# Kernel tuning notes

Hardware: AMD Instinct MI355X
Metric: run time of the kernel (lower is better)

## Reference

```python
import jax, jax.numpy as jnp
import numpy as np

B, N, C, D, H, O = 32, 2048, 16, 128, 128, 128


def setup_inputs():
    key = jax.random.key(0)
    ks = jax.random.split(key, 6)
    childrenList = jax.random.randint(ks[0], (B, N, C), 0, N)
    nodeEmb = jax.random.normal(ks[1], (B, N, D), dtype=jnp.float32)
    std1 = 1.0 / np.sqrt(D)
    W1 = jax.random.normal(ks[2], (3 * D, H), dtype=jnp.float32) * std1
    b1 = jax.random.normal(ks[3], (H,), dtype=jnp.float32) * (2.0 * std1)
    std2 = 1.0 / np.sqrt(H)
    W2 = jax.random.normal(ks[4], (H, O), dtype=jnp.float32) * std2
    b2 = jax.random.normal(ks[5], (O,), dtype=jnp.float32) * (2.0 * std2)
    return {"childrenList": childrenList, "nodeEmb": nodeEmb,
            "W1": W1, "b1": b1, "W2": W2, "b2": b2}


def _gather_feature(children, emb):
    # children: [B,N,C] int (0 = padding/no child), emb: [B,N,D]
    Bx, Nx, Dx = emb.shape
    # index 0 must look up a zero vector (padding child)
    lookup = jnp.concatenate([jnp.zeros((Bx, 1, Dx), emb.dtype), emb[:, 1:, :]], axis=1)
    child_emb = jax.vmap(lambda lu, ch: lu[ch])(lookup, children)      # [B,N,C,D]
    return jnp.concatenate([emb[:, :, None, :], child_emb], axis=2)    # [B,N,C+1,D]


def _conv_weights(children):
    # TBCNN positional coefficients eta_t / eta_r / eta_l (Mou et al.)
    Bx, Nx, Cx = children.shape
    f32 = jnp.float32
    mask = (children > 0).astype(f32)                                   # [B,N,C]
    t = jnp.concatenate([jnp.ones((Bx, Nx, 1), f32),
                         jnp.zeros((Bx, Nx, Cx), f32)], axis=2)        # parent=1, children=0
    num_sib = jnp.sum(mask, axis=2, keepdims=True)                      # [B,N,1]
    pos = jnp.arange(1, Cx + 1, dtype=f32)                              # 1-based child position
    r_child = jnp.where(num_sib == 1, 0.5 * mask,
                        mask * (pos - 1.0) / jnp.maximum(num_sib - 1.0, 1.0))
    r = jnp.concatenate([jnp.zeros((Bx, Nx, 1), f32), r_child], axis=2)
    full_mask = jnp.concatenate([jnp.ones((Bx, Nx, 1), f32), mask], axis=2)
    l = (1.0 - t) * (1.0 - r) * full_mask
    return jnp.stack([t, r, l], axis=-1)                                # [B,N,C+1,3]


def reference(childrenList, nodeEmb, W1, b1, W2, b2):
    feature = _gather_feature(childrenList, nodeEmb)                    # [B,N,C+1,D]
    weights = _conv_weights(childrenList)                               # [B,N,C+1,3]
    wf = jnp.einsum('bnck,bncd->bnkd', weights, feature)                # [B,N,3,D]
    wf = wf.reshape(wf.shape[0], wf.shape[1], -1)                       # [B,N,3D]
    h = jnp.tanh(wf @ W1 + b1)                                          # [B,N,H]
    pooled = jnp.max(h, axis=1)                                         # [B,H] max-pool over nodes
    out = jnp.tanh(pooled @ W2 + b2)                                    # [B,O]
    half = out.shape[0] // 2
    v1, v2 = out[:half], out[half:]
    eps = 1e-8
    n1 = jnp.maximum(jnp.linalg.norm(v1, axis=1), eps)
    n2 = jnp.maximum(jnp.linalg.norm(v2, axis=1), eps)
    return jnp.sum(v1 * v2, axis=1) / (n1 * n2)                         # [B/2]
```

## Files before the change

kernel.cpp:

```cpp
#include <hip/hip_runtime.h>

#define NB 32
#define NN 2048
#define NC 16
#define ND 128
#define NH 128
#define TM 64
#define NBLK (NB * (NN / TM))

typedef __bf16 bf16x8 __attribute__((ext_vector_type(8)));
typedef float f32x4 __attribute__((ext_vector_type(4)));
typedef float f32x2 __attribute__((ext_vector_type(2)));

__device__ __forceinline__ unsigned short f2bf(float f){
  unsigned u = __float_as_uint(f);
  u = (u + 0x7fffu + ((u >> 16) & 1u)) >> 16;
  return (unsigned short)u;
}
__device__ __forceinline__ unsigned enc_f32(float x){
  unsigned u = __float_as_uint(x);
  return (u & 0x80000000u) ? ~u : (u | 0x80000000u);
}
__device__ __forceinline__ float dec_f32(unsigned u){
  return __uint_as_float((u & 0x80000000u) ? (u & 0x7fffffffu) : ~u);
}
__device__ __forceinline__ unsigned pack4f8(float a, float b, float c, float d){
  int r = __builtin_amdgcn_cvt_pk_fp8_f32(a, b, 0, false);
  r = __builtin_amdgcn_cvt_pk_fp8_f32(c, d, r, true);
  return (unsigned)r;
}

__device__ __forceinline__ void stq(unsigned char* base, int stride, int row, int koff, uint4 u){
  *(uint4*)(base + row * stride + (koff ^ ((row & 7) << 4))) = u;
}
__device__ __forceinline__ void st8(unsigned char* base, int stride, int row, int koff, const float* f){
  uint4 u;
  u.x = (unsigned)f2bf(f[0]) | ((unsigned)f2bf(f[1]) << 16);
  u.y = (unsigned)f2bf(f[2]) | ((unsigned)f2bf(f[3]) << 16);
  u.z = (unsigned)f2bf(f[4]) | ((unsigned)f2bf(f[5]) << 16);
  u.w = (unsigned)f2bf(f[6]) | ((unsigned)f2bf(f[7]) << 16);
  stq(base, stride, row, koff, u);
}
__device__ __forceinline__ void st8p(unsigned char* base, int stride, int row, int koff, const f32x2* p){
  uint4 u;
  u.x = (unsigned)f2bf(p[0][0]) | ((unsigned)f2bf(p[0][1]) << 16);
  u.y = (unsigned)f2bf(p[1][0]) | ((unsigned)f2bf(p[1][1]) << 16);
  u.z = (unsigned)f2bf(p[2][0]) | ((unsigned)f2bf(p[2][1]) << 16);
  u.w = (unsigned)f2bf(p[3][0]) | ((unsigned)f2bf(p[3][1]) << 16);
  stq(base, stride, row, koff, u);
}
__device__ __forceinline__ uint4 ldq(const unsigned char* base, int stride, int row, int koff){
  return *(const uint4*)(base + row * stride + (koff ^ ((row & 7) << 4)));
}

#define OFF_POOLED 0
#define OFF_W1     16384
#define OFF_W2     114688
#define OFF_EMB    147456
#define WS_NEED_F8 (OFF_EMB + (size_t)NB*NN*ND)

__global__ __launch_bounds__(256) void tbcnn_prep(
    const float* __restrict__ nodeEmb, const float* __restrict__ W1,
    const float* __restrict__ W2, unsigned* __restrict__ pooled,
    uint4* __restrict__ w1frag, uint4* __restrict__ w2frag,
    unsigned char* __restrict__ embF8, int doEmb)
{
  const int blk = blockIdx.x;
  const int t = threadIdx.x;
  if (blk < 2048){
    if (!doEmb) return;
    const int chk = ((blk & 7) << 8) | (blk >> 3);
    const int tid = chk * 256 + t;
    const float4* src = (const float4*)nodeEmb;
    float4 v0 = src[tid * 4 + 0];
    float4 v1 = src[tid * 4 + 1];
    float4 v2 = src[tid * 4 + 2];
    float4 v3 = src[tid * 4 + 3];
    uint4 o;
    o.x = pack4f8(v0.x, v0.y, v0.z, v0.w);
    o.y = pack4f8(v1.x, v1.y, v1.z, v1.w);
    o.z = pack4f8(v2.x, v2.y, v2.z, v2.w);
    o.w = pack4f8(v3.x, v3.y, v3.z, v3.w);
    ((uint4*)embF8)[tid] = o;
  } else if (blk < 2072){
    const int tt = (blk - 2048) * 256 + t;
    if (tt < NB * NH) pooled[tt] = 0u;
    const int lane = tt & 63;
    const int rest = tt >> 6;
    const int ks = rest % 12;
    const int cf = rest / 12;
    const int col = (cf >> 1) * 32 + (cf & 1) * 16 + (lane & 15);
    const int k0 = ks * 32 + (lane >> 4) * 8;
    unsigned ps[4];
    #pragma unroll
    for (int p = 0; p < 4; ++p){
      unsigned lo = f2bf(W1[(size_t)(k0 + 2*p) * NH + col]);
      unsigned hi = f2bf(W1[(size_t)(k0 + 2*p + 1) * NH + col]);
      ps[p] = lo | (hi << 16);
    }
    w1frag[tt] = make_uint4(ps[0], ps[1], ps[2], ps[3]);
  } else {
    const int tt = (blk - 2072) * 256 + t;
    const int lane = tt & 63;
    const int rest = tt >> 6;
    const int ks = rest & 3;
    const int cf = rest >> 2;
    const int col = (cf >> 1) * 32 + (cf & 1) * 16 + (lane & 15);
    const int k0 = ks * 32 + (lane >> 4) * 8;
    unsigned ps[4];
    #pragma unroll
    for (int p = 0; p < 4; ++p){
      unsigned lo = f2bf(W2[(size_t)(k0 + 2*p) * NH + col]);
      unsigned hi = f2bf(W2[(size_t)(k0 + 2*p + 1) * NH + col]);
      ps[p] = lo | (hi << 16);
    }
    w2frag[tt] = make_uint4(ps[0], ps[1], ps[2], ps[3]);
  }
}

#define PROCF8(u, p) { \
  f32x2 lo_ = __builtin_amdgcn_cvt_pk_f32_fp8((int)(u), false); \
  f32x2 hi_ = __builtin_amdgcn_cvt_pk_f32_fp8((int)(u), true); \
  aR2[(p)]   += w_r * lo_; aL2[(p)]   += w_l * lo_; \
  aR2[(p)+1] += w_r * hi_; aL2[(p)+1] += w_l * hi_; }

#define ISSUE4(vv, D) { \
  D[0] = *(const uint4*)(embF8 + (rowbase + (unsigned)(vv).x) * ND + d0); \
  D[1] = *(const uint4*)(embF8 + (rowbase + (unsigned)(vv).y) * ND + d0); \
  D[2] = *(const uint4*)(embF8 + (rowbase + (unsigned)(vv).z) * ND + d0); \
  D[3] = *(const uint4*)(embF8 + (rowbase + (unsigned)(vv).w) * ND + d0); }

#define CW(c, idx) \
  const float mk  = ((idx) > 0) ? 1.0f : 0.0f; \
  const float wrc = one_sib ? (0.5f * mk) : (mk * (float)(c) * rdiv); \
  const float wlc = (1.0f - wrc) * mk; \
  const f32x2 w_r = (f32x2){wrc, wrc}; \
  const f32x2 w_l = (f32x2){wlc, wlc};

#define PROC4(g, vv, U) { \
  { CW(4*(g)+0, (vv).x) PROCF8(U[0].x,0) PROCF8(U[0].y,2) PROCF8(U[0].z,4) PROCF8(U[0].w,6) } \
  { CW(4*(g)+1, (vv).y) PROCF8(U[1].x,0) PROCF8(U[1].y,2) PROCF8(U[1].z,4) PROCF8(U[1].w,6) } \
  { CW(4*(g)+2, (vv).z) PROCF8(U[2].x,0) PROCF8(U[2].y,2) PROCF8(U[2].z,4) PROCF8(U[2].w,6) } \
  { CW(4*(g)+3, (vv).w) PROCF8(U[3].x,0) PROCF8(U[3].y,2) PROCF8(U[3].z,4) PROCF8(U[3].w,6) } }

template<bool F8>
__global__ __launch_bounds__(256, 2) void tbcnn_main(
    const int* __restrict__ children, const float* __restrict__ nodeEmb,
    const unsigned char* __restrict__ embF8, const uint4* __restrict__ w1frag,
    unsigned* __restrict__ pooled)
{
  __shared__ __align__(16) unsigned char wf_raw[TM * 768];
  const int j0 = ((blockIdx.x & 7) << 7) | (blockIdx.x >> 3);
  const int b = j0 >> 5;
  const int n0 = (j0 & 31) * TM;
  const int t = threadIdx.x;
  const int lane = t & 63;
  const int w = t >> 6;
  const size_t rowbase = (size_t)b * NN;

  #pragma unroll
  for (int pass = 0; pass < 2; ++pass){
    const int nloc = pass * 32 + (t >> 3);
    const int q = t & 7;
    const int d0 = q * 16;
    const int gn = n0 + nloc;
    const int4* chp4 = (const int4*)(children + (rowbase + gn) * NC);

    const int4 vA = chp4[0], vB = chp4[1], vC = chp4[2], vD = chp4[3];
    int ns = (vA.x > 0) + (vA.y > 0) + (vA.z > 0) + (vA.w > 0)
           + (vB.x > 0) + (vB.y > 0) + (vB.z > 0) + (vB.w > 0)
           + (vC.x > 0) + (vC.y > 0) + (vC.z > 0) + (vC.w > 0)
           + (vD.x > 0) + (vD.y > 0) + (vD.z > 0) + (vD.w > 0);
    const float rdiv = 1.0f / (float)(((ns - 1) > 1) ? (ns - 1) : 1);
    const bool one_sib = (ns == 1);

    if (F8){
      f32x2 aR2[8], aL2[8];
      #pragma unroll
      for (int i = 0; i < 8; ++i){ aR2[i] = (f32x2){0.f,0.f}; aL2[i] = (f32x2){0.f,0.f}; }

      uint4 g0[4], g1[4];
      const uint4 sq = *(const uint4*)(embF8 + (rowbase + gn) * ND + d0);
      ISSUE4(vA, g0)
      ISSUE4(vB, g1)
      __builtin_amdgcn_sched_barrier(0);
      {
        f32x2 sv[8];
        sv[0] = __builtin_amdgcn_cvt_pk_f32_fp8((int)sq.x, false);
        sv[1] = __builtin_amdgcn_cvt_pk_f32_fp8((int)sq.x, true);
        sv[2] = __builtin_amdgcn_cvt_pk_f32_fp8((int)sq.y, false);
        sv[3] = __builtin_amdgcn_cvt_pk_f32_fp8((int)sq.y, true);
        sv[4] = __builtin_amdgcn_cvt_pk_f32_fp8((int)sq.z, false);
        sv[5] = __builtin_amdgcn_cvt_pk_f32_fp8((int)sq.z, true);
        sv[6] = __builtin_amdgcn_cvt_pk_f32_fp8((int)sq.w, false);
        sv[7] = __builtin_amdgcn_cvt_pk_f32_fp8((int)sq.w, true);
        st8p(wf_raw, 768, nloc, 2 * d0,       sv);
        st8p(wf_raw, 768, nloc, 2 * (d0 + 8), sv + 4);
      }
      PROC4(0, vA, g0)
      ISSUE4(vC, g0)
      __builtin_amdgcn_sched_barrier(0);
      PROC4(1, vB, g1)
      ISSUE4(vD, g1)
      __builtin_amdgcn_sched_barrier(0);
      PROC4(2, vC, g0)
      __builtin_amdgcn_sched_barrier(0);
      PROC4(3, vD, g1)

      st8p(wf_raw, 768, nloc, 2 * (ND + d0),         aR2);
      st8p(wf_raw, 768, nloc, 2 * (ND + d0 + 8),     aR2 + 4);
      st8p(wf_raw, 768, nloc, 2 * (2 * ND + d0),     aL2);
      st8p(wf_raw, 768, nloc, 2 * (2 * ND + d0 + 8), aL2 + 4);
    } else {
      const float* sp = nodeEmb + (rowbase + gn) * ND + d0;
      float sv[16];
      #pragma unroll
      for (int j = 0; j < 4; ++j){
        float4 s = *(const float4*)(sp + j * 4);
        sv[j*4+0]=s.x; sv[j*4+1]=s.y; sv[j*4+2]=s.z; sv[j*4+3]=s.w;
      }
      st8(wf_raw, 768, nloc, 2 * d0, sv);
      st8(wf_raw, 768, nloc, 2 * (d0 + 8), sv + 8);
      float aR[16], aL[16];
      #pragma unroll
      for (int i = 0; i < 16; ++i){ aR[i] = 0.0f; aL[i] = 0.0f; }
      const int4 vs[4] = {vA, vB, vC, vD};
      #pragma unroll
      for (int c4 = 0; c4 < 4; ++c4){
        int cidx[4] = {vs[c4].x, vs[c4].y, vs[c4].z, vs[c4].w};
        #pragma unroll
        for (int jj = 0; jj < 4; ++jj){
          const int c = c4 * 4 + jj;
          const int idx = cidx[jj];
          const float mk  = (idx > 0) ? 1.0f : 0.0f;
          const float wrc = one_sib ? (0.5f * mk) : (mk * (float)c * rdiv);
          const float wlc = (1.0f - wrc) * mk;
          const float* cp = nodeEmb + (rowbase + idx) * ND + d0;
          #pragma unroll
          for (int j = 0; j < 4; ++j){
            float4 u = *(const float4*)(cp + j * 4);
            aR[j*4+0] += wrc * u.x; aL[j*4+0] += wlc * u.x;
            aR[j*4+1] += wrc * u.y; aL[j*4+1] += wlc * u.y;
            aR[j*4+2] += wrc * u.z; aL[j*4+2] += wlc * u.z;
            aR[j*4+3] += wrc * u.w; aL[j*4+3] += wlc * u.w;
          }
        }
      }
      st8(wf_raw, 768, nloc, 2 * (ND + d0),         aR);
      st8(wf_raw, 768, nloc, 2 * (ND + d0 + 8),     aR + 8);
      st8(wf_raw, 768, nloc, 2 * (2 * ND + d0),     aL);
      st8(wf_raw, 768, nloc, 2 * (2 * ND + d0 + 8), aL + 8);
    }
  }
  __syncthreads();

  {
    f32x4 acc[4][2];
    #pragma unroll
    for (int rf = 0; rf < 4; ++rf){
      acc[rf][0] = (f32x4){0.f, 0.f, 0.f, 0.f};
      acc[rf][1] = (f32x4){0.f, 0.f, 0.f, 0.f};
    }
    #pragma unroll 4
    for (int ks = 0; ks < 12; ++ks){
      bf16x8 B0 = __builtin_bit_cast(bf16x8, w1frag[((w * 2 + 0) * 12 + ks) * 64 + lane]);
      bf16x8 B1 = __builtin_bit_cast(bf16x8, w1frag[((w * 2 + 1) * 12 + ks) * 64 + lane]);
      const int koff = ks * 64 + ((lane >> 4) << 4);
      #pragma unroll
      for (int rf = 0; rf < 4; ++rf){
        const int row = rf * 16 + (lane & 15);
        bf16x8 a = __builtin_bit_cast(bf16x8, ldq(wf_raw, 768, row, koff));
        acc[rf][0] = __builtin_amdgcn_mfma_f32_16x16x32_bf16(a, B0, acc[rf][0], 0, 0, 0);
        acc[rf][1] = __builtin_amdgcn_mfma_f32_16x16x32_bf16(a, B1, acc[rf][1], 0, 0, 0);
      }
    }

    float m0 = -3.0e38f, m1 = -3.0e38f;
    #pragma unroll
    for (int rf = 0; rf < 4; ++rf)
      #pragma unroll
      for (int i = 0; i < 4; ++i){
        m0 = fmaxf(m0, acc[rf][0][i]);
        m1 = fmaxf(m1, acc[rf][1][i]);
      }
    m0 = fmaxf(m0, __shfl_xor(m0, 16, 64));
    m0 = fmaxf(m0, __shfl_xor(m0, 32, 64));
    m1 = fmaxf(m1, __shfl_xor(m1, 16, 64));
    m1 = fmaxf(m1, __shfl_xor(m1, 32, 64));
    if (lane < 16){
      atomicMax(pooled + b * NH + w * 32 + lane,      enc_f32(m0));
      atomicMax(pooled + b * NH + w * 32 + 16 + lane, enc_f32(m1));
    }
  }
}

__global__ __launch_bounds__(256) void tbcnn_final(
    const unsigned* __restrict__ pooled, const float* __restrict__ b1,
    const uint4* __restrict__ w2frag, const float* __restrict__ b2,
    float* __restrict__ out)
{
  __shared__ __align__(16) unsigned char hls[NB * 256];
  __shared__ float os[NB * NH];
  const int t = threadIdx.x;
  const int lane = t & 63;
  const int w = t >> 6;

  {
    const int row = t >> 3;
    const int q = t & 7;
    const int d0 = q * 16;
    const unsigned* pp = pooled + row * NH + d0;
    const float* bp = b1 + d0;
    float hv[16];
    #pragma unroll
    for (int j = 0; j < 16; ++j) hv[j] = tanhf(dec_f32(pp[j]) + bp[j]);
    st8(hls, 256, row, 2 * d0, hv);
    st8(hls, 256, row, 2 * (d0 + 8), hv + 8);
  }
  __syncthreads();
  {
    f32x4 acc[2][2];
    #pragma unroll
    for (int rf = 0; rf < 2; ++rf){
      acc[rf][0] = (f32x4){0.f,0.f,0.f,0.f};
      acc[rf][1] = (f32x4){0.f,0.f,0.f,0.f};
    }
    #pragma unroll
    for (int ks = 0; ks < 4; ++ks){
      bf16x8 B0 = __builtin_bit_cast(bf16x8, w2frag[((w * 2 + 0) * 4 + ks) * 64 + lane]);
      bf16x8 B1 = __builtin_bit_cast(bf16x8, w2frag[((w * 2 + 1) * 4 + ks) * 64 + lane]);
      const int koff = ks * 64 + ((lane >> 4) << 4);
      #pragma unroll
      for (int rf = 0; rf < 2; ++rf){
        bf16x8 a = __builtin_bit_cast(bf16x8, ldq(hls, 256, rf * 16 + (lane & 15), koff));
        acc[rf][0] = __builtin_amdgcn_mfma_f32_16x16x32_bf16(a, B0, acc[rf][0], 0, 0, 0);
        acc[rf][1] = __builtin_amdgcn_mfma_f32_16x16x32_bf16(a, B1, acc[rf][1], 0, 0, 0);
      }
    }
    #pragma unroll
    for (int rf = 0; rf < 2; ++rf)
      #pragma unroll
      for (int cf = 0; cf < 2; ++cf){
        const int col = w * 32 + cf * 16 + (lane & 15);
        const float bias = b2[col];
        #pragma unroll
        for (int i = 0; i < 4; ++i){
          const int r = rf * 16 + (lane >> 4) * 4 + i;
          os[r * NH + col] = tanhf(acc[rf][cf][i] + bias);
        }
      }
  }
  __syncthreads();
  if (t < 16){
    float s12 = 0.f, s11 = 0.f, s22 = 0.f;
    #pragma unroll 4
    for (int d = 0; d < NH; ++d){
      float a = os[t * NH + d];
      float c = os[(t + 16) * NH + d];
      s12 += a * c; s11 += a * a; s22 += c * c;
    }
    float n1 = fmaxf(sqrtf(s11), 1e-8f);
    float n2 = fmaxf(sqrtf(s22), 1e-8f);
    out[t] = s12 / (n1 * n2);
  }
}

extern "C" void kernel_launch(void* const* d_in, const int* in_sizes, int n_in,
                              void* d_out, int out_size, void* d_ws, size_t ws_size,
                              hipStream_t stream)
{
  const int*   children = (const int*)d_in[0];
  const float* nodeEmb  = (const float*)d_in[1];
  const float* W1       = (const float*)d_in[2];
  const float* b1       = (const float*)d_in[3];
  const float* W2       = (const float*)d_in[4];
  const float* b2       = (const float*)d_in[5];
  float* out = (float*)d_out;

  unsigned* pooled      = (unsigned*)((char*)d_ws + OFF_POOLED);
  uint4* w1frag         = (uint4*)((char*)d_ws + OFF_W1);
  uint4* w2frag         = (uint4*)((char*)d_ws + OFF_W2);
  unsigned char* embF8  = (unsigned char*)((char*)d_ws + OFF_EMB);

  const bool f8 = (ws_size >= WS_NEED_F8);

  tbcnn_prep<<<2080, 256, 0, stream>>>(nodeEmb, W1, W2, pooled, w1frag, w2frag, embF8, f8 ? 1 : 0);
  if (f8)
    tbcnn_main<true><<<NBLK, 256, 0, stream>>>(children, nodeEmb, embF8, w1frag, pooled);
  else
    tbcnn_main<false><<<NBLK, 256, 0, stream>>>(children, nodeEmb, embF8, w1frag, pooled);
  tbcnn_final<<<1, 256, 0, stream>>>(pooled, b1, w2frag, b2, out);
}
```

Baseline: 40.91 us.

## Use 512-thread blocks so each node row and each output tile gets its own thread/wave

Doubles the block size of the main kernel from 256 to 512 threads. The two-pass gather loop becomes a single pass, with each thread handling one node-row slice. The MFMA stage now uses 8 waves that each compute one 16-column output slice instead of 4 waves computing two. This aims to expose more parallelism and latency hiding within a block, but launch bounds drop to one block per CU and per-thread register pressure changes.

After: 41.26 us. Within noise of the previous version (+0.9%).

```diff
diff --git a/kernel.cpp b/kernel.cpp
--- a/kernel.cpp
+++ b/kernel.cpp
@@ -144,7 +144,7 @@
   { CW(4*(g)+3, (vv).w) PROCF8(U[3].x,0) PROCF8(U[3].y,2) PROCF8(U[3].z,4) PROCF8(U[3].w,6) } }
 
 template<bool F8>
-__global__ __launch_bounds__(256, 2) void tbcnn_main(
+__global__ __launch_bounds__(512, 1) void tbcnn_main(
     const int* __restrict__ children, const float* __restrict__ nodeEmb,
     const unsigned char* __restrict__ embF8, const uint4* __restrict__ w1frag,
     unsigned* __restrict__ pooled)
@@ -158,9 +158,8 @@
   const int w = t >> 6;
   const size_t rowbase = (size_t)b * NN;
 
-  #pragma unroll
-  for (int pass = 0; pass < 2; ++pass){
-    const int nloc = pass * 32 + (t >> 3);
+  {
+    const int nloc = t >> 3;
     const int q = t & 7;
     const int d0 = q * 16;
     const int gn = n0 + nloc;
@@ -255,42 +254,31 @@
   __syncthreads();
 
   {
-    f32x4 acc[4][2];
-    #pragma unroll
-    for (int rf = 0; rf < 4; ++rf){
-      acc[rf][0] = (f32x4){0.f, 0.f, 0.f, 0.f};
-      acc[rf][1] = (f32x4){0.f, 0.f, 0.f, 0.f};
-    }
+    f32x4 acc[4];
+    #pragma unroll
+    for (int rf = 0; rf < 4; ++rf) acc[rf] = (f32x4){0.f, 0.f, 0.f, 0.f};
     #pragma unroll 4
     for (int ks = 0; ks < 12; ++ks){
-      bf16x8 B0 = __builtin_bit_cast(bf16x8, w1frag[((w * 2 + 0) * 12 + ks) * 64 + lane]);
-      bf16x8 B1 = __builtin_bit_cast(bf16x8, w1frag[((w * 2 + 1) * 12 + ks) * 64 + lane]);
+      bf16x8 B0 = __builtin_bit_cast(bf16x8, w1frag[(w * 12 + ks) * 64 + lane]);
       const int koff = ks * 64 + ((lane >> 4) << 4);
       #pragma unroll
       for (int rf = 0; rf < 4; ++rf){
         const int row = rf * 16 + (lane & 15);
         bf16x8 a = __builtin_bit_cast(bf16x8, ldq(wf_raw, 768, row, koff));
-        acc[rf][0] = __builtin_amdgcn_mfma_f32_16x16x32_bf16(a, B0, acc[rf][0], 0, 0, 0);
-        acc[rf][1] = __builtin_amdgcn_mfma_f32_16x16x32_bf16(a, B1, acc[rf][1], 0, 0, 0);
-      }
-    }
-
-    float m0 = -3.0e38f, m1 = -3.0e38f;
+        acc[rf] = __builtin_amdgcn_mfma_f32_16x16x32_bf16(a, B0, acc[rf], 0, 0, 0);
+      }
+    }
+
+    float m0 = -3.0e38f;
     #pragma unroll
     for (int rf = 0; rf < 4; ++rf)
       #pragma unroll
-      for (int i = 0; i < 4; ++i){
-        m0 = fmaxf(m0, acc[rf][0][i]);
-        m1 = fmaxf(m1, acc[rf][1][i]);
-      }
+      for (int i = 0; i < 4; ++i)
+        m0 = fmaxf(m0, acc[rf][i]);
     m0 = fmaxf(m0, __shfl_xor(m0, 16, 64));
     m0 = fmaxf(m0, __shfl_xor(m0, 32, 64));
-    m1 = fmaxf(m1, __shfl_xor(m1, 16, 64));
-    m1 = fmaxf(m1, __shfl_xor(m1, 32, 64));
-    if (lane < 16){
-      atomicMax(pooled + b * NH + w * 32 + lane,      enc_f32(m0));
-      atomicMax(pooled + b * NH + w * 32 + 16 + lane, enc_f32(m1));
-    }
+    if (lane < 16)
+      atomicMax(pooled + b * NH + w * 16 + lane, enc_f32(m0));
   }
 }
 
@@ -386,8 +374,8 @@
 
   tbcnn_prep<<<2080, 256, 0, stream>>>(nodeEmb, W1, W2, pooled, w1frag, w2frag, embF8, f8 ? 1 : 0);
   if (f8)
-    tbcnn_main<true><<<NBLK, 256, 0, stream>>>(children, nodeEmb, embF8, w1frag, pooled);
+    tbcnn_main<true><<<NBLK, 512, 0, stream>>>(children, nodeEmb, embF8, w1frag, pooled);
   else
-    tbcnn_main<false><<<NBLK, 256, 0, stream>>>(children, nodeEmb, embF8, w1frag, pooled);
+    tbcnn_main<false><<<NBLK, 512, 0, stream>>>(children, nodeEmb, embF8, w1frag, pooled);
   tbcnn_final<<<1, 256, 0, stream>>>(pooled, b1, w2frag, b2, out);
 }
```

## Overlap first-half MFMA with second-half gather in FP8 path

Applied to the files above, without the earlier changes.

Splits the gather phase into two halves separated by a barrier, then runs the MFMAs for the first 32 rows interleaved with the global gather loads and FP8 conversion work for the second 32 rows. The remaining MFMAs for rows 32-63 follow after a second barrier. The goal is to hide gather memory latency behind matrix work inside each block. It adds an extra __syncthreads and raises register pressure from holding accumulators live through the gather.

Result: slower. 42.80 us (+4.6%).

```diff
diff --git a/kernel.cpp b/kernel.cpp
--- a/kernel.cpp
+++ b/kernel.cpp
@@ -143,6 +143,30 @@
   { CW(4*(g)+2, (vv).z) PROCF8(U[2].x,0) PROCF8(U[2].y,2) PROCF8(U[2].z,4) PROCF8(U[2].w,6) } \
   { CW(4*(g)+3, (vv).w) PROCF8(U[3].x,0) PROCF8(U[3].y,2) PROCF8(U[3].z,4) PROCF8(U[3].w,6) } }
 
+#define SELF_STORE(SQ, ROW) { \
+  f32x2 sv[8]; \
+  sv[0] = __builtin_amdgcn_cvt_pk_f32_fp8((int)(SQ).x, false); \
+  sv[1] = __builtin_amdgcn_cvt_pk_f32_fp8((int)(SQ).x, true); \
+  sv[2] = __builtin_amdgcn_cvt_pk_f32_fp8((int)(SQ).y, false); \
+  sv[3] = __builtin_amdgcn_cvt_pk_f32_fp8((int)(SQ).y, true); \
+  sv[4] = __builtin_amdgcn_cvt_pk_f32_fp8((int)(SQ).z, false); \
+  sv[5] = __builtin_amdgcn_cvt_pk_f32_fp8((int)(SQ).z, true); \
+  sv[6] = __builtin_amdgcn_cvt_pk_f32_fp8((int)(SQ).w, false); \
+  sv[7] = __builtin_amdgcn_cvt_pk_f32_fp8((int)(SQ).w, true); \
+  st8p(wf_raw, 768, (ROW), 2 * d0,       sv); \
+  st8p(wf_raw, 768, (ROW), 2 * (d0 + 8), sv + 4); }
+
+#define MFMA01(KS) { \
+  bf16x8 B0_ = __builtin_bit_cast(bf16x8, w1frag[((w * 2 + 0) * 12 + (KS)) * 64 + lane]); \
+  bf16x8 B1_ = __builtin_bit_cast(bf16x8, w1frag[((w * 2 + 1) * 12 + (KS)) * 64 + lane]); \
+  const int koff_ = (KS) * 64 + ((lane >> 4) << 4); \
+  bf16x8 a0_ = __builtin_bit_cast(bf16x8, ldq(wf_raw, 768, (lane & 15),      koff_)); \
+  bf16x8 a1_ = __builtin_bit_cast(bf16x8, ldq(wf_raw, 768, 16 + (lane & 15), koff_)); \
+  acc[0][0] = __builtin_amdgcn_mfma_f32_16x16x32_bf16(a0_, B0_, acc[0][0], 0, 0, 0); \
+  acc[0][1] = __builtin_amdgcn_mfma_f32_16x16x32_bf16(a0_, B1_, acc[0][1], 0, 0, 0); \
+  acc[1][0] = __builtin_amdgcn_mfma_f32_16x16x32_bf16(a1_, B0_, acc[1][0], 0, 0, 0); \
+  acc[1][1] = __builtin_amdgcn_mfma_f32_16x16x32_bf16(a1_, B1_, acc[1][1], 0, 0, 0); }
+
 template<bool F8>
 __global__ __launch_bounds__(256, 2) void tbcnn_main(
     const int* __restrict__ children, const float* __restrict__ nodeEmb,
@@ -157,46 +181,38 @@
   const int lane = t & 63;
   const int w = t >> 6;
   const size_t rowbase = (size_t)b * NN;
-
+  const int q = t & 7;
+  const int d0 = q * 16;
+
+  f32x4 acc[4][2];
   #pragma unroll
-  for (int pass = 0; pass < 2; ++pass){
-    const int nloc = pass * 32 + (t >> 3);
-    const int q = t & 7;
-    const int d0 = q * 16;
-    const int gn = n0 + nloc;
-    const int4* chp4 = (const int4*)(children + (rowbase + gn) * NC);
-
-    const int4 vA = chp4[0], vB = chp4[1], vC = chp4[2], vD = chp4[3];
-    int ns = (vA.x > 0) + (vA.y > 0) + (vA.z > 0) + (vA.w > 0)
-           + (vB.x > 0) + (vB.y > 0) + (vB.z > 0) + (vB.w > 0)
-           + (vC.x > 0) + (vC.y > 0) + (vC.z > 0) + (vC.w > 0)
-           + (vD.x > 0) + (vD.y > 0) + (vD.z > 0) + (vD.w > 0);
-    const float rdiv = 1.0f / (float)(((ns - 1) > 1) ? (ns - 1) : 1);
-    const bool one_sib = (ns == 1);
-
-    if (F8){
+  for (int rf = 0; rf < 4; ++rf){
+    acc[rf][0] = (f32x4){0.f, 0.f, 0.f, 0.f};
+    acc[rf][1] = (f32x4){0.f, 0.f, 0.f, 0.f};
+  }
+
+  if (F8){
+    {
+      const int nloc = t >> 3;
+      const int gn = n0 + nloc;
+      const int4* chp4 = (const int4*)(children + (rowbase + gn) * NC);
+      const int4 vA = chp4[0], vB = chp4[1], vC = chp4[2], vD = chp4[3];
+      int ns = (vA.x > 0) + (vA.y > 0) + (vA.z > 0) + (vA.w > 0)
+             + (vB.x > 0) + (vB.y > 0) + (vB.z > 0) + (vB.w > 0)
+             + (vC.x > 0) + (vC.y > 0) + (vC.z > 0) + (vC.w > 0)
+             + (vD.x > 0) + (vD.y > 0) + (vD.z > 0) + (vD.w > 0);
+      const float rdiv = 1.0f / (float)(((ns - 1) > 1) ? (ns - 1) : 1);
+      const bool one_sib = (ns == 1);
+
       f32x2 aR2[8], aL2[8];
       #pragma unroll
       for (int i = 0; i < 8; ++i){ aR2[i] = (f32x2){0.f,0.f}; aL2[i] = (f32x2){0.f,0.f}; }
-
       uint4 g0[4], g1[4];
       const uint4 sq = *(const uint4*)(embF8 + (rowbase + gn) * ND + d0);
       ISSUE4(vA, g0)
       ISSUE4(vB, g1)
       __builtin_amdgcn_sched_barrier(0);
-      {
-        f32x2 sv[8];
-        sv[0] = __builtin_amdgcn_cvt_pk_f32_fp8((int)sq.x, false);
-        sv[1] = __builtin_amdgcn_cvt_pk_f32_fp8((int)sq.x, true);
-        sv[2] = __builtin_amdgcn_cvt_pk_f32_fp8((int)sq.y, false);
-        sv[3] = __builtin_amdgcn_cvt_pk_f32_fp8((int)sq.y, true);
-        sv[4] = __builtin_amdgcn_cvt_pk_f32_fp8((int)sq.z, false);
-        sv[5] = __builtin_amdgcn_cvt_pk_f32_fp8((int)sq.z, true);
-        sv[6] = __builtin_amdgcn_cvt_pk_f32_fp8((int)sq.w, false);
-        sv[7] = __builtin_amdgcn_cvt_pk_f32_fp8((int)sq.w, true);
-        st8p(wf_raw, 768, nloc, 2 * d0,       sv);
-        st8p(wf_raw, 768, nloc, 2 * (d0 + 8), sv + 4);
-      }
+      SELF_STORE(sq, nloc)
       PROC4(0, vA, g0)
       ISSUE4(vC, g0)
       __builtin_amdgcn_sched_barrier(0);
@@ -206,12 +222,80 @@
       PROC4(2, vC, g0)
       __builtin_amdgcn_sched_barrier(0);
       PROC4(3, vD, g1)
-
       st8p(wf_raw, 768, nloc, 2 * (ND + d0),         aR2);
       st8p(wf_raw, 768, nloc, 2 * (ND + d0 + 8),     aR2 + 4);
       st8p(wf_raw, 768, nloc, 2 * (2 * ND + d0),     aL2);
       st8p(wf_raw, 768, nloc, 2 * (2 * ND + d0 + 8), aL2 + 4);
-    } else {
+    }
+    __syncthreads();
+
+    {
+      const int nloc = 32 + (t >> 3);
+      const int gn = n0 + nloc;
+      const int4* chp4 = (const int4*)(children + (rowbase + gn) * NC);
+      const int4 vA = chp4[0], vB = chp4[1], vC = chp4[2], vD = chp4[3];
+      int ns = (vA.x > 0) + (vA.y > 0) + (vA.z > 0) + (vA.w > 0)
+             + (vB.x > 0) + (vB.y > 0) + (vB.z > 0) + (vB.w > 0)
+             + (vC.x > 0) + (vC.y > 0) + (vC.z > 0) + (vC.w > 0)
+             + (vD.x > 0) + (vD.y > 0) + (vD.z > 0) + (vD.w > 0);
+      const float rdiv = 1.0f / (float)(((ns - 1) > 1) ? (ns - 1) : 1);
+      const bool one_sib = (ns == 1);
+
+      f32x2 aR2[8], aL2[8];
+      #pragma unroll
+      for (int i = 0; i < 8; ++i){ aR2[i] = (f32x2){0.f,0.f}; aL2[i] = (f32x2){0.f,0.f}; }
+      uint4 g0[4], g1[4];
+      const uint4 sq = *(const uint4*)(embF8 + (rowbase + gn) * ND + d0);
+      ISSUE4(vA, g0)
+      ISSUE4(vB, g1)
+      __builtin_amdgcn_sched_barrier(0);
+      MFMA01(0) MFMA01(1) MFMA01(2) MFMA01(3) MFMA01(4) MFMA01(5)
+      __builtin_amdgcn_sched_barrier(0);
+      SELF_STORE(sq, nloc)
+      PROC4(0, vA, g0)
+      ISSUE4(vC, g0)
+      __builtin_amdgcn_sched_barrier(0);
+      MFMA01(6) MFMA01(7) MFMA01(8) MFMA01(9) MFMA01(10) MFMA01(11)
+      __builtin_amdgcn_sched_barrier(0);
+      PROC4(1, vB, g1)
+      ISSUE4(vD, g1)
+      __builtin_amdgcn_sched_barrier(0);
+      PROC4(2, vC, g0)
+      __builtin_amdgcn_sched_barrier(0);
+      PROC4(3, vD, g1)
+      st8p(wf_raw, 768, nloc, 2 * (ND + d0),         aR2);
+      st8p(wf_raw, 768, nloc, 2 * (ND + d0 + 8),     aR2 + 4);
+      st8p(wf_raw, 768, nloc, 2 * (2 * ND + d0),     aL2);
+      st8p(wf_raw, 768, nloc, 2 * (2 * ND + d0 + 8), aL2 + 4);
+    }
+    __syncthreads();
+
+    #pragma unroll 4
+    for (int ks = 0; ks < 12; ++ks){
+      bf16x8 B0 = __builtin_bit_cast(bf16x8, w1frag[((w * 2 + 0) * 12 + ks) * 64 + lane]);
+      bf16x8 B1 = __builtin_bit_cast(bf16x8, w1frag[((w * 2 + 1) * 12 + ks) * 64 + lane]);
+      const int koff = ks * 64 + ((lane >> 4) << 4);
+      #pragma unroll
+      for (int rf = 2; rf < 4; ++rf){
+        const int row = rf * 16 + (lane & 15);
+        bf16x8 a = __builtin_bit_cast(bf16x8, ldq(wf_raw, 768, row, koff));
+        acc[rf][0] = __builtin_amdgcn_mfma_f32_16x16x32_bf16(a, B0, acc[rf][0], 0, 0, 0);
+        acc[rf][1] = __builtin_amdgcn_mfma_f32_16x16x32_bf16(a, B1, acc[rf][1], 0, 0, 0);
+      }
+    }
+  } else {
+    #pragma unroll
+    for (int pass = 0; pass < 2; ++pass){
+      const int nloc = pass * 32 + (t >> 3);
+      const int gn = n0 + nloc;
+      const int4* chp4 = (const int4*)(children + (rowbase + gn) * NC);
+      const int4 vA = chp4[0], vB = chp4[1], vC = chp4[2], vD = chp4[3];
+      int ns = (vA.x > 0) + (vA.y > 0) + (vA.z > 0) + (vA.w > 0)
+             + (vB.x > 0) + (vB.y > 0) + (vB.z > 0) + (vB.w > 0)
+             + (vC.x > 0) + (vC.y > 0) + (vC.z > 0) + (vC.w > 0)
+             + (vD.x > 0) + (vD.y > 0) + (vD.z > 0) + (vD.w > 0);
+      const float rdiv = 1.0f / (float)(((ns - 1) > 1) ? (ns - 1) : 1);
+      const bool one_sib = (ns == 1);
       const float* sp = nodeEmb + (rowbase + gn) * ND + d0;
       float sv[16];
       #pragma unroll
@@ -251,16 +335,7 @@
       st8(wf_raw, 768, nloc, 2 * (2 * ND + d0),     aL);
       st8(wf_raw, 768, nloc, 2 * (2 * ND + d0 + 8), aL + 8);
     }
-  }
-  __syncthreads();
-
-  {
-    f32x4 acc[4][2];
-    #pragma unroll
-    for (int rf = 0; rf < 4; ++rf){
-      acc[rf][0] = (f32x4){0.f, 0.f, 0.f, 0.f};
-      acc[rf][1] = (f32x4){0.f, 0.f, 0.f, 0.f};
-    }
+    __syncthreads();
     #pragma unroll 4
     for (int ks = 0; ks < 12; ++ks){
       bf16x8 B0 = __builtin_bit_cast(bf16x8, w1frag[((w * 2 + 0) * 12 + ks) * 64 + lane]);
@@ -274,7 +349,9 @@
         acc[rf][1] = __builtin_amdgcn_mfma_f32_16x16x32_bf16(a, B1, acc[rf][1], 0, 0, 0);
       }
     }
-
+  }
+
+  {
     float m0 = -3.0e38f, m1 = -3.0e38f;
     #pragma unroll
     for (int rf = 0; rf < 4; ++rf)
```
